# Kernel optimization log

Hardware: AMD Instinct MI355X
Metric: run time of the kernel (lower is better)

## Reference

```python
import jax, jax.numpy as jnp
import numpy as np

RES = 32          # resolution (32, 32) -> N = 1024 tokens
HEADS = 16
EMB = 1024
BATCH = 8
N = RES * RES


def _bias_idxs(res):
    # relative-offset index table, [N, N] with values in [0, res*res)
    coords = np.stack(np.meshgrid(np.arange(res), np.arange(res), indexing='ij'), -1).reshape(-1, 2)
    d = np.abs(coords[:, None, :] - coords[None, :, :])  # [N, N, 2]
    return jnp.asarray(d[..., 0] * res + d[..., 1], dtype=jnp.int64)


def setup_inputs() -> dict:
    key = jax.random.key(0)
    k1, k2, k3, k4, k5 = jax.random.split(key, 5)
    x = jax.random.normal(k1, (BATCH, N, EMB), dtype=jnp.float32)
    w_qkv = jax.random.normal(k2, (3 * EMB, EMB), dtype=jnp.float32) * 0.02
    biases = jax.random.normal(k3, (HEADS, RES * RES), dtype=jnp.float32) * 0.02
    bias_idxs = _bias_idxs(RES)
    w_out = jax.random.normal(k4, (EMB, EMB), dtype=jnp.float32) * 0.02
    b_out = jax.random.normal(k5, (EMB,), dtype=jnp.float32) * 0.02
    return {"x": x, "w_qkv": w_qkv, "biases": biases,
            "bias_idxs": bias_idxs, "w_out": w_out, "b_out": b_out}


def reference(x, w_qkv, biases, bias_idxs, w_out, b_out):
    b, n, e = x.shape
    h = HEADS
    d = e // h
    scale = d ** -0.5
    # to_qkv: Linear(e, 3e, bias=False); torch Linear computes x @ W.T
    qkv = x @ w_qkv.T                                   # [b, n, 3e]
    q, k, v = jnp.split(qkv, 3, axis=-1)
    def to_heads(t):
        return t.reshape(b, n, h, d).transpose(0, 2, 1, 3)  # b h n d
    q, k, v = to_heads(q), to_heads(k), to_heads(v)
    scores = jnp.einsum('bhid,bhjd->bhij', q, k) * scale    # [b, h, n, n]
    scores = scores + biases[:, bias_idxs]                  # gather -> [h, n, n], broadcast over b
    attn = jax.nn.softmax(scores, axis=-1)
    out = jnp.einsum('bhij,bhjd->bhid', attn, v)            # [b, h, n, d]
    out = out.transpose(0, 2, 1, 3).reshape(b, n, e)        # b n (h d)
    # to_out: Linear(e, e) with bias (dropout = identity at inference)
    return out @ w_out.T + b_out
```

## Files before the change

kernel.cpp:

```cpp
#include <hip/hip_runtime.h>
#include <stdint.h>


#define LOG2E 1.4426950408889634f
#define QSCL 0.18033688011112042f

typedef __attribute__((ext_vector_type(8))) short short8;
typedef __attribute__((ext_vector_type(4))) short short4v;
typedef __attribute__((ext_vector_type(4))) float floatx4;
typedef __attribute__((ext_vector_type(2))) unsigned int uint2v;

__device__ __forceinline__ short f2bf(float f) {
  uint32_t u = __builtin_bit_cast(uint32_t, f);
  u = (u + 0x7FFFu + ((u >> 16) & 1u)) >> 16;
  return (short)(uint16_t)u;
}
__device__ __forceinline__ float bf2f(short s) {
  uint32_t u = ((uint32_t)(uint16_t)s) << 16;
  return __builtin_bit_cast(float, u);
}
__device__ __forceinline__ float fast_exp2(float x) {
#if __has_builtin(__builtin_amdgcn_exp2f)
  return __builtin_amdgcn_exp2f(x);
#else
  return exp2f(x);
#endif
}

__device__ __forceinline__ void gload_lds16(const short* g, short* l) {
  __builtin_amdgcn_global_load_lds(
      (const __attribute__((address_space(1))) void*)g,
      (__attribute__((address_space(3))) void*)l, 16, 0, 0);
}

__global__ void prep(const float* __restrict__ x, const float* __restrict__ wqkv,
                     const float* __restrict__ wout, const float* __restrict__ biases,
                     short* __restrict__ xb, short* __restrict__ wqkvb,
                     short* __restrict__ woutb, short* __restrict__ biast) {
  int blk = blockIdx.x, tid = threadIdx.x;
  if (blk < 12288) {
    const float* src;
    short* dst;
    int i;
    if (blk < 8192) { src = x; dst = xb; i = blk * 256 + tid; }
    else if (blk < 11264) { src = wqkv; dst = wqkvb; i = (blk - 8192) * 256 + tid; }
    else { src = wout; dst = woutb; i = (blk - 11264) * 256 + tid; }
    float4 f = ((const float4*)src)[i];
    short4v o;
    o.x = f2bf(f.x); o.y = f2bf(f.y); o.z = f2bf(f.z); o.w = f2bf(f.w);
    ((short4v*)dst)[i] = o;
  } else {
    int tile = (blk - 12288) * 4 + (tid >> 6);
    int lane = tid & 63, qd = lane >> 4, col = lane & 15;
    int bp = tile & 1, ap = (tile >> 1) & 1, dra = (tile >> 2) & 31, h = tile >> 7;
    int ci = 16 * bp + col;
    short4v o;
#pragma unroll
    for (int r = 0; r < 4; r++) {
      int cj = 16 * ap + 4 * qd + r;
      int dc = cj - ci; if (dc < 0) dc = -dc;
      o[r] = f2bf(biases[h * 1024 + dra * 32 + dc] * LOG2E);
    }
    *(short4v*)&biast[(size_t)tile * 256 + lane * 4] = o;
  }
}

template <int MODE>
__global__ __launch_bounds__(256, 2) void gemm_bt(
    const short* __restrict__ A, const short* __restrict__ Bt,
    short* __restrict__ qo, short* __restrict__ ko, short* __restrict__ vto,
    const float* __restrict__ bvec, float* __restrict__ outf) {
  __shared__ __align__(16) short sA[128 * 64];
  __shared__ __align__(16) short sB[128 * 64];
  const int tid = threadIdx.x;
  const int w = tid >> 6, lane = tid & 63;
  const int wr = w >> 1, wc = w & 1;
  const int bm = blockIdx.y, bn = blockIdx.x;
  const int qd = lane >> 4, col = lane & 15;

  floatx4 acc[4][4] = {};
  const int rowA0 = bm * 128, rowB0 = bn * 128;
  const int ciw = w * 256;

  for (int kk = 0; kk < 1024; kk += 64) {
    __syncthreads();
#pragma unroll
    for (int n = 0; n < 4; n++) {
      int ci = ciw + n * 64 + lane;
      int r = ci >> 3, c = (ci & 7) ^ (r & 7);
      gload_lds16(A + (size_t)(rowA0 + r) * 1024 + kk + c * 8, &sA[ci * 8]);
    }
#pragma unroll
    for (int n = 0; n < 4; n++) {
      int ci = ciw + n * 64 + lane;
      int r = ci >> 3, c = (ci & 7) ^ (r & 7);
      gload_lds16(Bt + (size_t)(rowB0 + r) * 1024 + kk + c * 8, &sB[ci * 8]);
    }
    __syncthreads();

#pragma unroll
    for (int ks = 0; ks < 2; ks++) {
      const int ch = qd + ks * 4;
      short8 af[4], bff[4];
#pragma unroll
      for (int rt = 0; rt < 4; rt++) {
        int r = wr * 64 + rt * 16 + col;
        af[rt] = *(const short8*)&sA[r * 64 + ((ch ^ (r & 7)) << 3)];
      }
#pragma unroll
      for (int ct = 0; ct < 4; ct++) {
        int r = wc * 64 + ct * 16 + col;
        bff[ct] = *(const short8*)&sB[r * 64 + ((ch ^ (r & 7)) << 3)];
      }
#pragma unroll
      for (int rt = 0; rt < 4; rt++)
#pragma unroll
        for (int ct = 0; ct < 4; ct++)
          acc[rt][ct] = __builtin_amdgcn_mfma_f32_16x16x32_bf16(af[rt], bff[ct], acc[rt][ct], 0, 0, 0);
    }
  }

  if (MODE == 0) {
    if (bn >= 16) {
#pragma unroll
      for (int rt = 0; rt < 4; rt++) {
#pragma unroll
        for (int ct = 0; ct < 4; ct++) {
          int Cg = bn * 128 + wc * 64 + ct * 16 + col;
          int e = Cg & 1023, h = e >> 6, dd = e & 63;
          short4v pv;
#pragma unroll
          for (int r = 0; r < 4; r++) pv[r] = f2bf(acc[rt][ct][r]);
          int R0 = bm * 128 + wr * 64 + rt * 16 + qd * 4;
          int b = R0 >> 10, n0 = R0 & 1023;
          int bh = b * 16 + h;
          *(short4v*)&vto[((size_t)bh * 64 + dd) * 1024 + n0] = pv;
        }
      }
    } else {
#pragma unroll
      for (int rt = 0; rt < 4; rt++) {
#pragma unroll
        for (int ct = 0; ct < 4; ct++) {
          int Cg = bn * 128 + wc * 64 + ct * 16 + col;
          int which = Cg >> 10, e = Cg & 1023, h = e >> 6, dd = e & 63;
#pragma unroll
          for (int r = 0; r < 4; r++) {
            int R = bm * 128 + wr * 64 + rt * 16 + qd * 4 + r;
            int b = R >> 10, n = R & 1023;
            int bh = b * 16 + h;
            float av = acc[rt][ct][r];
            if (which == 0) av *= QSCL;
            short v = f2bf(av);
            if (which == 0)
              qo[((size_t)bh * 1024 + n) * 64 + dd] = v;
            else
              ko[((size_t)bh * 1024 + n) * 64 + dd] = v;
          }
        }
      }
    }
  } else {
#pragma unroll
    for (int rt = 0; rt < 4; rt++)
#pragma unroll
      for (int ct = 0; ct < 4; ct++) {
        int Cg = bn * 128 + wc * 64 + ct * 16 + col;
        float bo = bvec[Cg];
#pragma unroll
        for (int r = 0; r < 4; r++) {
          int R = bm * 128 + wr * 64 + rt * 16 + qd * 4 + r;
          outf[(size_t)R * 1024 + Cg] = acc[rt][ct][r] + bo;
        }
      }
  }
}

__global__ __launch_bounds__(256, 3) void attn_fused(
    const short* __restrict__ q, const short* __restrict__ k,
    const short* __restrict__ vt, const short* __restrict__ biast,
    short* __restrict__ ao) {
  __shared__ __align__(16) short sK[128 * 64];
  __shared__ __align__(16) short sVt[64 * 128];
  __shared__ __align__(16) short sP[64 * 128];
  const int tid = threadIdx.x, w = tid >> 6, lane = tid & 63;
  const int bh = blockIdx.x, qt = blockIdx.y;
  const int h = bh & 15;
  const int qd = lane >> 4, col = lane & 15;
  const short* qb = q + (size_t)bh * 65536;
  const short* kb = k + (size_t)bh * 65536;
  const short* vb = vt + (size_t)bh * 65536;
  const int ciw = w * 256;

#pragma unroll
  for (int n = 0; n < 2; n++) {
    int ci = w * 128 + n * 64 + lane;
    int r = ci >> 3, c = (ci & 7) ^ (r & 7);
    gload_lds16(qb + (size_t)(qt * 64 + r) * 64 + c * 8, &sP[ci * 8]);
  }
  __syncthreads();
  short8 bq[2][4];
#pragma unroll
  for (int ks = 0; ks < 2; ks++) {
    const int ch = qd + ks * 4;
#pragma unroll
    for (int ct = 0; ct < 4; ct++) {
      int r2 = ct * 16 + col;
      bq[ks][ct] = *(const short8*)&sP[r2 * 64 + ((ch ^ (r2 & 7)) << 3)];
    }
  }

  short8 onesf;
#pragma unroll
  for (int t = 0; t < 8; t++) onesf[t] = (short)0x3F80;

  floatx4 oacc[4] = {};
  floatx4 osum = {};

  for (int js = 0; js < 8; js++) {
    __syncthreads();

    short4v bfrag[2][4];
#pragma unroll
    for (int rt = 0; rt < 2; rt++) {
      const int a = js * 8 + w * 2 + rt;
      const int ar = a >> 1, ap = a & 1;
#pragma unroll
      for (int ct = 0; ct < 4; ct++) {
        int b = qt * 4 + ct;
        int dra = ar - (b >> 1); if (dra < 0) dra = -dra;
        int tile = ((h * 32 + dra) * 2 + ap) * 2 + (b & 1);
        bfrag[rt][ct] = *(const short4v*)&biast[(size_t)tile * 256 + lane * 4];
      }
    }

#pragma unroll
    for (int n = 0; n < 4; n++) {
      int ci = ciw + n * 64 + lane;
      int r = ci >> 3, c = (ci & 7) ^ (r & 7);
      gload_lds16(kb + (size_t)(js * 128 + r) * 64 + c * 8, &sK[ci * 8]);
    }
#pragma unroll
    for (int n = 0; n < 4; n++) {
      int ci = ciw + n * 64 + lane;
      int r = ci >> 4, c = (ci & 15) ^ (r & 15);
      gload_lds16(vb + (size_t)r * 1024 + js * 128 + c * 8, &sVt[ci * 8]);
    }
    __syncthreads();

#pragma unroll
    for (int rt = 0; rt < 2; rt++) {
      const int s = w * 8 + rt * 4 + qd;
      const int r = w * 32 + rt * 16 + col;
      short8 ak0 = *(const short8*)&sK[r * 64 + (((qd + 0) ^ (r & 7)) << 3)];
      short8 ak1 = *(const short8*)&sK[r * 64 + (((qd + 4) ^ (r & 7)) << 3)];
      floatx4 sacc[4];
#pragma unroll
      for (int ct = 0; ct < 4; ct++) {
        sacc[ct][0] = bf2f(bfrag[rt][ct][0]);
        sacc[ct][1] = bf2f(bfrag[rt][ct][1]);
        sacc[ct][2] = bf2f(bfrag[rt][ct][2]);
        sacc[ct][3] = bf2f(bfrag[rt][ct][3]);
      }
      __builtin_amdgcn_s_setprio(1);
#pragma unroll
      for (int ct = 0; ct < 4; ct++)
        sacc[ct] = __builtin_amdgcn_mfma_f32_16x16x32_bf16(ak0, bq[0][ct], sacc[ct], 0, 0, 0);
#pragma unroll
      for (int ct = 0; ct < 4; ct++)
        sacc[ct] = __builtin_amdgcn_mfma_f32_16x16x32_bf16(ak1, bq[1][ct], sacc[ct], 0, 0, 0);
      __builtin_amdgcn_s_setprio(0);
#pragma unroll
      for (int ct = 0; ct < 4; ct++) {
        int i = ct * 16 + col;
        float e0 = fast_exp2(sacc[ct][0]);
        float e1 = fast_exp2(sacc[ct][1]);
        float e2 = fast_exp2(sacc[ct][2]);
        float e3 = fast_exp2(sacc[ct][3]);
        uint32_t u0 = __builtin_bit_cast(uint32_t, e0) + 0x8000u;
        uint32_t u1 = __builtin_bit_cast(uint32_t, e1) + 0x8000u;
        uint32_t u2 = __builtin_bit_cast(uint32_t, e2) + 0x8000u;
        uint32_t u3 = __builtin_bit_cast(uint32_t, e3) + 0x8000u;
        uint2v pk;
        pk.x = __builtin_amdgcn_perm(u1, u0, 0x07060302u);
        pk.y = __builtin_amdgcn_perm(u3, u2, 0x07060302u);
        *(uint2v*)&sP[i * 128 + ((s ^ (i & 15)) << 2)] = pk;
      }
    }
    __syncthreads();

#pragma unroll
    for (int ks = 0; ks < 4; ks++) {
      const int ch = ks * 4 + qd;
      int m = w * 16 + col;
      short4v lo = *(const short4v*)&sP[m * 128 + (((2 * ch) ^ col) << 2)];
      short4v hi = *(const short4v*)&sP[m * 128 + (((2 * ch + 1) ^ col) << 2)];
      short8 ap = __builtin_shufflevector(lo, hi, 0, 1, 2, 3, 4, 5, 6, 7);
      short8 bv[4];
#pragma unroll
      for (int ct = 0; ct < 4; ct++) {
        int d = ct * 16 + col;
        bv[ct] = *(const short8*)&sVt[d * 128 + ((ch ^ (d & 15)) << 3)];
      }
      __builtin_amdgcn_s_setprio(1);
#pragma unroll
      for (int ct = 0; ct < 4; ct++)
        oacc[ct] = __builtin_amdgcn_mfma_f32_16x16x32_bf16(ap, bv[ct], oacc[ct], 0, 0, 0);
      osum = __builtin_amdgcn_mfma_f32_16x16x32_bf16(ap, onesf, osum, 0, 0, 0);
      __builtin_amdgcn_s_setprio(0);
    }
  }

  const int b = bh >> 4;
  floatx4 inv;
#pragma unroll
  for (int r = 0; r < 4; r++) inv[r] = 1.0f / osum[r];
#pragma unroll
  for (int ct = 0; ct < 4; ct++)
#pragma unroll
    for (int r = 0; r < 4; r++) {
      int n = qt * 64 + w * 16 + qd * 4 + r;
      int dd = ct * 16 + col;
      ao[(((size_t)b * 1024 + n) << 10) + h * 64 + dd] = f2bf(oacc[ct][r] * inv[r]);
    }
}

extern "C" void kernel_launch(void* const* d_in, const int* in_sizes, int n_in,
                              void* d_out, int out_size, void* d_ws, size_t ws_size,
                              hipStream_t stream) {
  const float* x = (const float*)d_in[0];
  const float* w_qkv = (const float*)d_in[1];
  const float* biases = (const float*)d_in[2];
  const float* w_out = (const float*)d_in[4];
  const float* b_out = (const float*)d_in[5];
  float* out = (float*)d_out;

  char* ws = (char*)d_ws;
  short* xb    = (short*)(ws + 0);
  short* wqkvb = (short*)(ws + 16777216);
  short* woutb = (short*)(ws + 23068672);
  short* qb    = (short*)(ws + 25165824);
  short* kb    = (short*)(ws + 41943040);
  short* vtb   = (short*)(ws + 58720256);
  short* aob   = (short*)(ws + 75497472);
  short* biast = (short*)(ws + 92274688);

  prep<<<13312, 256, 0, stream>>>(x, w_qkv, w_out, biases, xb, wqkvb, woutb, biast);
  gemm_bt<0><<<dim3(24, 64), 256, 0, stream>>>(xb, wqkvb, qb, kb, vtb, nullptr, nullptr);
  attn_fused<<<dim3(128, 16), 256, 0, stream>>>(qb, kb, vtb, biast, aob);
  gemm_bt<1><<<dim3(8, 64), 256, 0, stream>>>(aob, woutb, nullptr, nullptr, nullptr, b_out, out);
}
```

Before: 250.8 us.

## Prefetch next K/V tile into registers during compute in attention loop

Preloads the first K and V^T tiles before the loop, then on each iteration issues global loads for the next tile into registers, runs the compute, and writes the registers to LDS after a barrier. This is meant to hide global-memory latency behind the MFMA work instead of stalling on direct-to-LDS loads at the start of each iteration. It costs 32 extra VGPRs per thread, which can lower occupancy under launch_bounds(256,3), and adds an extra barrier per iteration.

```diff
diff --git a/kernel.cpp b/kernel.cpp
--- a/kernel.cpp
+++ b/kernel.cpp
@@ -9,6 +9,7 @@
 typedef __attribute__((ext_vector_type(4))) short short4v;
 typedef __attribute__((ext_vector_type(4))) float floatx4;
 typedef __attribute__((ext_vector_type(2))) unsigned int uint2v;
+typedef __attribute__((ext_vector_type(4))) int int4v;
 
 __device__ __forceinline__ short f2bf(float f) {
   uint32_t u = __builtin_bit_cast(uint32_t, f);
@@ -192,13 +193,29 @@
   const short* vb = vt + (size_t)bh * 65536;
   const int ciw = w * 256;
 
+  int kci[4], kr[4], kc[4], vr[4], vc[4];
+#pragma unroll
+  for (int n = 0; n < 4; n++) {
+    int ci = ciw + n * 64 + lane;
+    kci[n] = ci;
+    kr[n] = ci >> 3; kc[n] = (ci & 7) ^ (kr[n] & 7);
+    vr[n] = ci >> 4; vc[n] = (ci & 15) ^ (vr[n] & 15);
+  }
+
 #pragma unroll
   for (int n = 0; n < 2; n++) {
     int ci = w * 128 + n * 64 + lane;
     int r = ci >> 3, c = (ci & 7) ^ (r & 7);
     gload_lds16(qb + (size_t)(qt * 64 + r) * 64 + c * 8, &sP[ci * 8]);
   }
+#pragma unroll
+  for (int n = 0; n < 4; n++)
+    gload_lds16(kb + (size_t)kr[n] * 64 + kc[n] * 8, &sK[kci[n] * 8]);
+#pragma unroll
+  for (int n = 0; n < 4; n++)
+    gload_lds16(vb + (size_t)vr[n] * 1024 + vc[n] * 8, &sVt[kci[n] * 8]);
   __syncthreads();
+
   short8 bq[2][4];
 #pragma unroll
   for (int ks = 0; ks < 2; ks++) {
@@ -209,6 +226,7 @@
       bq[ks][ct] = *(const short8*)&sP[r2 * 64 + ((ch ^ (r2 & 7)) << 3)];
     }
   }
+  __syncthreads();
 
   short8 onesf;
 #pragma unroll
@@ -218,7 +236,15 @@
   floatx4 osum = {};
 
   for (int js = 0; js < 8; js++) {
-    __syncthreads();
+    int4v kreg[4], vreg[4];
+    if (js < 7) {
+#pragma unroll
+      for (int n = 0; n < 4; n++)
+        kreg[n] = *(const int4v*)(kb + (size_t)((js + 1) * 128 + kr[n]) * 64 + kc[n] * 8);
+#pragma unroll
+      for (int n = 0; n < 4; n++)
+        vreg[n] = *(const int4v*)(vb + (size_t)vr[n] * 1024 + (js + 1) * 128 + vc[n] * 8);
+    }
 
     short4v bfrag[2][4];
 #pragma unroll
@@ -233,20 +259,6 @@
         bfrag[rt][ct] = *(const short4v*)&biast[(size_t)tile * 256 + lane * 4];
       }
     }
-
-#pragma unroll
-    for (int n = 0; n < 4; n++) {
-      int ci = ciw + n * 64 + lane;
-      int r = ci >> 3, c = (ci & 7) ^ (r & 7);
-      gload_lds16(kb + (size_t)(js * 128 + r) * 64 + c * 8, &sK[ci * 8]);
-    }
-#pragma unroll
-    for (int n = 0; n < 4; n++) {
-      int ci = ciw + n * 64 + lane;
-      int r = ci >> 4, c = (ci & 15) ^ (r & 15);
-      gload_lds16(vb + (size_t)r * 1024 + js * 128 + c * 8, &sVt[ci * 8]);
-    }
-    __syncthreads();
 
 #pragma unroll
     for (int rt = 0; rt < 2; rt++) {
@@ -309,6 +321,15 @@
       osum = __builtin_amdgcn_mfma_f32_16x16x32_bf16(ap, onesf, osum, 0, 0, 0);
       __builtin_amdgcn_s_setprio(0);
     }
+    __syncthreads();
+
+    if (js < 7) {
+#pragma unroll
+      for (int n = 0; n < 4; n++) *(int4v*)&sK[kci[n] * 8] = kreg[n];
+#pragma unroll
+      for (int n = 0; n < 4; n++) *(int4v*)&sVt[kci[n] * 8] = vreg[n];
+      __syncthreads();
+    }
   }
 
   const int b = bh >> 4;
```

After: 258.7 us. 3.2% more time.
